# Kernel optimization log

Hardware: AMD Instinct MI355X
Metric: run time of the kernel (lower is better)

## Reference

```python
import jax, jax.numpy as jnp
import numpy as np

D_MODEL = 4096
RANK = 16
BATCH = 4
SEQ = 4096


def setup_inputs() -> dict:
    key = jax.random.key(0)
    k_x, k_w, k_b, k_a, k_bb = jax.random.split(key, 5)
    x = jax.random.normal(k_x, (BATCH, SEQ, D_MODEL), dtype=jnp.float32)
    W = jax.random.normal(k_w, (D_MODEL, D_MODEL), dtype=jnp.float32) * 0.02
    bias = jax.random.normal(k_b, (D_MODEL,), dtype=jnp.float32) * 0.02
    A = jax.random.normal(k_a, (D_MODEL, RANK), dtype=jnp.float32) * 0.01
    B = jax.random.normal(k_bb, (RANK, D_MODEL), dtype=jnp.float32) * 0.01
    return {"x": x, "W": W, "bias": bias, "A": A, "B": B}


def reference(x, W, bias, A, B):
    # Faithful to the torch module: delta_W = A @ B; linear(x, W + delta_W, bias)
    # i.e. out = x @ (W + A @ B)^T + bias, with W: [d_out, d_in], x: [b, s, d_in].
    delta_W = A @ B                                   # [d_out, d_in]
    out = jnp.einsum("bsi,oi->bso", x, W + delta_W) + bias
    return out
```

## Files before the change

kernel.cpp:

```cpp
#include <hip/hip_runtime.h>
#include <stdint.h>


#define MDIM 16384
#define NDIM 4096
#define KDIM 4096
#define RANK 16
#define NT   (KDIM / 64)

typedef __bf16  bf16x8 __attribute__((ext_vector_type(8)));
typedef float   f32x4  __attribute__((ext_vector_type(4)));
typedef unsigned short u16x8 __attribute__((ext_vector_type(8)));

__device__ __forceinline__ unsigned short f2bf(float f) {
  union { float f; uint32_t u; } v; v.f = f;
  uint32_t r = v.u + 0x7FFFu + ((v.u >> 16) & 1u);
  return (unsigned short)(r >> 16);
}

__device__ __forceinline__ void gl16(const void* g, void* l) {
  __builtin_amdgcn_global_load_lds(
      (__attribute__((address_space(1))) void*)(g),
      (__attribute__((address_space(3))) void*)(l),
      16, 0, 0);
}

__global__ void prep_w(const float* __restrict__ W, const float* __restrict__ A,
                       const float* __restrict__ Bm, unsigned short* __restrict__ Wp) {
  const int i = blockIdx.x * 256 + threadIdx.x;
  const int o = blockIdx.y;
  float acc = W[(size_t)o * NDIM + i];
#pragma unroll
  for (int r = 0; r < RANK; ++r)
    acc += A[o * RANK + r] * Bm[(size_t)r * NDIM + i];
  Wp[(size_t)o * NDIM + i] = f2bf(acc);
}

__global__ void cast_x(const float* __restrict__ x, unsigned short* __restrict__ xb) {
  const size_t i = ((size_t)blockIdx.x * 256 + threadIdx.x) * 8;
  float4 a = *(const float4*)(x + i);
  float4 b = *(const float4*)(x + i + 4);
  u16x8 o;
  o[0] = f2bf(a.x); o[1] = f2bf(a.y); o[2] = f2bf(a.z); o[3] = f2bf(a.w);
  o[4] = f2bf(b.x); o[5] = f2bf(b.y); o[6] = f2bf(b.z); o[7] = f2bf(b.w);
  *(u16x8*)(xb + i) = o;
}

#define BARRIER  __builtin_amdgcn_s_barrier()
#define VMCNT8   asm volatile("s_waitcnt vmcnt(8)" ::: "memory")
#define VMCNT6   asm volatile("s_waitcnt vmcnt(6)" ::: "memory")
#define WAITVM0  asm volatile("s_waitcnt vmcnt(0)" ::: "memory")

#define STAGE_A(buf, h, kt) do {                                              \
    const int kc_ = ((kt) < NT ? (kt) : NT - 1);                              \
    const unsigned short* g_ = agb + (size_t)((h) * 64) * KDIM + kc_ * 64;    \
    unsigned short* d_ = &sA[(buf)][0] + (h) * 8192 + t * 8;                  \
    gl16(g_, d_);                                                             \
    gl16(g_ + (size_t)128 * KDIM, d_ + 4096);                                 \
  } while (0)

#define STAGE_B(buf, h, kt) do {                                              \
    const int kc_ = ((kt) < NT ? (kt) : NT - 1);                              \
    const unsigned short* g_ = bgb + (size_t)((h) * 32) * KDIM + kc_ * 64;    \
    unsigned short* d_ = &sB[(buf)][0] + (h) * 8192 + t * 8;                  \
    gl16(g_, d_);                                                             \
    gl16(g_ + (size_t)128 * KDIM, d_ + 4096);                                 \
  } while (0)

#define LDA(buf, mh) do {                                                     \
    _Pragma("unroll") for (int mi = 0; mi < 4; ++mi)                          \
    _Pragma("unroll") for (int kk = 0; kk < 2; ++kk)                          \
      a[mi][kk] = *(const bf16x8*)(saw + (buf)*16384 + ((mh)*128 + mi*16)*64  \
                                   + ((kk*32 + koff) ^ xorE));                \
  } while (0)

#define LDB(buf, nh, bb) do {                                                 \
    _Pragma("unroll") for (int ni = 0; ni < 2; ++ni)                          \
    _Pragma("unroll") for (int kk = 0; kk < 2; ++kk)                          \
      bb[ni][kk] = *(const bf16x8*)(sbw + (buf)*16384 + ((nh)*128 + ni*16)*64 \
                                    + ((kk*32 + koff) ^ xorE));               \
  } while (0)

#define MM(mh, nh, bb) do {                                                   \
    __builtin_amdgcn_s_setprio(1);                                            \
    _Pragma("unroll") for (int mi = 0; mi < 4; ++mi)                          \
    _Pragma("unroll") for (int ni = 0; ni < 2; ++ni)                          \
    _Pragma("unroll") for (int kk = 0; kk < 2; ++kk)                          \
      acc[(mh)*4+mi][(nh)*2+ni] = __builtin_amdgcn_mfma_f32_16x16x32_bf16(    \
          a[mi][kk], bb[ni][kk], acc[(mh)*4+mi][(nh)*2+ni], 0, 0, 0);         \
    __builtin_amdgcn_s_setprio(0);                                            \
  } while (0)

__global__ __launch_bounds__(512, 2) void gemm256(
    const unsigned short* __restrict__ Xb,
    const unsigned short* __restrict__ Wp,
    const float* __restrict__ bias,
    float* __restrict__ out) {
  __shared__ __align__(16) unsigned short sA[2][256 * 64];
  __shared__ __align__(16) unsigned short sB[2][256 * 64];

  const int t  = threadIdx.x;
  const int l  = t & 63;
  const int w  = t >> 6;
  const int wm = w >> 2;
  const int wn = w & 3;

  const int bid = blockIdx.x;
  const int swz = (bid & 7) * (1024 / 8) + (bid >> 3);
  const int bm  = (swz >> 4) * 256;
  const int bn  = (swz & 15) * 256;

  const int sr  = t >> 3;
  const int ske = (((t & 7) * 16) ^ ((sr & 7) << 4)) >> 1;
  const unsigned short* agb = Xb + (size_t)(bm + sr) * KDIM + ske;
  const unsigned short* bgb = Wp + (size_t)(bn + (sr >> 5) * 64 + (sr & 31)) * KDIM + ske;

  const int lr   = l & 15;
  const int koff = (l >> 4) * 8;
  const int xorE = (lr & 7) << 3;
  const unsigned short* saw = &sA[0][0] + (wm * 64 + lr) * 64;
  const unsigned short* sbw = &sB[0][0] + (wn * 32 + lr) * 64;

  bf16x8 a[4][2], b0[2][2], b1[2][2];
  f32x4 acc[8][4];
#pragma unroll
  for (int i = 0; i < 8; ++i)
#pragma unroll
    for (int j = 0; j < 4; ++j)
      acc[i][j] = f32x4{0.f, 0.f, 0.f, 0.f};

  STAGE_A(0, 0, 0); STAGE_B(0, 0, 0); STAGE_A(0, 1, 0); STAGE_B(0, 1, 0);
  STAGE_A(1, 0, 1); STAGE_B(1, 0, 1); STAGE_B(1, 1, 1);
  VMCNT6;
  BARRIER;

  for (int it = 0; it < NT / 2; ++it) {
    const int E = it * 2;
    LDA(0, 0); LDB(0, 0, b0);
    STAGE_A(1, 1, E + 1);
    BARRIER;
    MM(0, 0, b0);
    BARRIER;
    LDB(0, 1, b1);
    STAGE_A(0, 0, E + 2);
    BARRIER;
    MM(0, 1, b1);
    VMCNT8;
    BARRIER;
    LDA(0, 1);
    STAGE_B(0, 0, E + 2);
    BARRIER;
    MM(1, 1, b1);
    BARRIER;
    STAGE_B(0, 1, E + 2);
    BARRIER;
    MM(1, 0, b0);
    VMCNT8;
    BARRIER;
    LDA(1, 0); LDB(1, 0, b0);
    STAGE_A(0, 1, E + 2);
    BARRIER;
    MM(0, 0, b0);
    BARRIER;
    LDB(1, 1, b1);
    STAGE_A(1, 0, E + 3);
    BARRIER;
    MM(0, 1, b1);
    VMCNT8;
    BARRIER;
    LDA(1, 1);
    STAGE_B(1, 0, E + 3);
    BARRIER;
    MM(1, 1, b1);
    BARRIER;
    STAGE_B(1, 1, E + 3);
    BARRIER;
    MM(1, 0, b0);
    VMCNT8;
    BARRIER;
  }

  WAITVM0;

#pragma unroll
  for (int mf = 0; mf < 8; ++mf) {
#pragma unroll
    for (int nf = 0; nf < 4; ++nf) {
      const int row = bm + wm * 128 + mf * 16 + (l >> 4) * 4;
      const int col = bn + wn * 64 + nf * 16 + lr;
      const float bv = bias[col];
#pragma unroll
      for (int r = 0; r < 4; ++r)
        out[(size_t)(row + r) * NDIM + col] = acc[mf][nf][r] + bv;
    }
  }
}

extern "C" void kernel_launch(void* const* d_in, const int* in_sizes, int n_in,
                              void* d_out, int out_size, void* d_ws, size_t ws_size,
                              hipStream_t stream) {
  const float* x    = (const float*)d_in[0];
  const float* W    = (const float*)d_in[1];
  const float* bias = (const float*)d_in[2];
  const float* A    = (const float*)d_in[3];
  const float* B    = (const float*)d_in[4];
  float* out        = (float*)d_out;

  unsigned short* Wp = (unsigned short*)d_ws;
  unsigned short* Xb = (unsigned short*)d_ws + (size_t)NDIM * KDIM;

  prep_w<<<dim3(NDIM / 256, NDIM), 256, 0, stream>>>(W, A, B, Wp);
  cast_x<<<dim3((size_t)MDIM * KDIM / (256 * 8)), 256, 0, stream>>>(x, Xb);
  gemm256<<<dim3((MDIM / 256) * (NDIM / 256)), 512, 0, stream>>>(Xb, Wp, bias, out);
}
```

Before: 634.1 us.

## Software-pipeline LDS fragment loads one quadrant ahead of MFMA with register double-buffering

Restructures the GEMM main loop so each shared-memory fragment load for the next quadrant is issued before the MFMA block that consumes the previous fragments. It uses extra register buffers (aA/aB, bX/bY/bZ) and sched_barriers, and re-times the global-to-LDS staging with uniform vmcnt(6) waits. The aim is to hide LDS read latency behind matrix math and remove the separate barrier-only phases. The cost is higher VGPR pressure, which may hurt occupancy under launch_bounds(512,2), plus some risk in the buffer-reuse ordering.

```diff
diff --git a/kernel.cpp b/kernel.cpp
--- a/kernel.cpp
+++ b/kernel.cpp
@@ -47,9 +47,10 @@
 }
 
 #define BARRIER  __builtin_amdgcn_s_barrier()
-#define VMCNT8   asm volatile("s_waitcnt vmcnt(8)" ::: "memory")
 #define VMCNT6   asm volatile("s_waitcnt vmcnt(6)" ::: "memory")
+#define VMCNT4   asm volatile("s_waitcnt vmcnt(4)" ::: "memory")
 #define WAITVM0  asm volatile("s_waitcnt vmcnt(0)" ::: "memory")
+#define SCHEDB   __builtin_amdgcn_sched_barrier(0)
 
 #define STAGE_A(buf, h, kt) do {                                              \
     const int kc_ = ((kt) < NT ? (kt) : NT - 1);                              \
@@ -67,27 +68,27 @@
     gl16(g_ + (size_t)128 * KDIM, d_ + 4096);                                 \
   } while (0)
 
-#define LDA(buf, mh) do {                                                     \
+#define LDA_TO(dst, buf, mh) do {                                             \
     _Pragma("unroll") for (int mi = 0; mi < 4; ++mi)                          \
     _Pragma("unroll") for (int kk = 0; kk < 2; ++kk)                          \
-      a[mi][kk] = *(const bf16x8*)(saw + (buf)*16384 + ((mh)*128 + mi*16)*64  \
-                                   + ((kk*32 + koff) ^ xorE));                \
-  } while (0)
-
-#define LDB(buf, nh, bb) do {                                                 \
+      dst[mi][kk] = *(const bf16x8*)(saw + (buf)*16384 + ((mh)*128 + mi*16)*64\
+                                     + ((kk*32 + koff) ^ xorE));              \
+  } while (0)
+
+#define LDB_TO(dst, buf, nh) do {                                             \
     _Pragma("unroll") for (int ni = 0; ni < 2; ++ni)                          \
     _Pragma("unroll") for (int kk = 0; kk < 2; ++kk)                          \
-      bb[ni][kk] = *(const bf16x8*)(sbw + (buf)*16384 + ((nh)*128 + ni*16)*64 \
-                                    + ((kk*32 + koff) ^ xorE));               \
-  } while (0)
-
-#define MM(mh, nh, bb) do {                                                   \
+      dst[ni][kk] = *(const bf16x8*)(sbw + (buf)*16384 + ((nh)*128 + ni*16)*64\
+                                     + ((kk*32 + koff) ^ xorE));              \
+  } while (0)
+
+#define MMQ(mh, nh, aS, bS) do {                                              \
     __builtin_amdgcn_s_setprio(1);                                            \
     _Pragma("unroll") for (int mi = 0; mi < 4; ++mi)                          \
     _Pragma("unroll") for (int ni = 0; ni < 2; ++ni)                          \
     _Pragma("unroll") for (int kk = 0; kk < 2; ++kk)                          \
       acc[(mh)*4+mi][(nh)*2+ni] = __builtin_amdgcn_mfma_f32_16x16x32_bf16(    \
-          a[mi][kk], bb[ni][kk], acc[(mh)*4+mi][(nh)*2+ni], 0, 0, 0);         \
+          aS[mi][kk], bS[ni][kk], acc[(mh)*4+mi][(nh)*2+ni], 0, 0, 0);        \
     __builtin_amdgcn_s_setprio(0);                                            \
   } while (0)
 
@@ -121,7 +122,7 @@
   const unsigned short* saw = &sA[0][0] + (wm * 64 + lr) * 64;
   const unsigned short* sbw = &sB[0][0] + (wn * 32 + lr) * 64;
 
-  bf16x8 a[4][2], b0[2][2], b1[2][2];
+  bf16x8 aA[4][2], aB[4][2], bX[2][2], bY[2][2], bZ[2][2];
   f32x4 acc[8][4];
 #pragma unroll
   for (int i = 0; i < 8; ++i)
@@ -129,55 +130,55 @@
     for (int j = 0; j < 4; ++j)
       acc[i][j] = f32x4{0.f, 0.f, 0.f, 0.f};
 
-  STAGE_A(0, 0, 0); STAGE_B(0, 0, 0); STAGE_A(0, 1, 0); STAGE_B(0, 1, 0);
-  STAGE_A(1, 0, 1); STAGE_B(1, 0, 1); STAGE_B(1, 1, 1);
-  VMCNT6;
+  STAGE_B(0, 0, 0); STAGE_A(0, 0, 0); STAGE_B(0, 1, 0); STAGE_A(0, 1, 0);
+  STAGE_B(1, 0, 1); STAGE_A(1, 0, 1);
+  VMCNT4;
   BARRIER;
+  LDB_TO(bX, 0, 0);
+  LDA_TO(aA, 0, 0);
 
   for (int it = 0; it < NT / 2; ++it) {
     const int E = it * 2;
-    LDA(0, 0); LDB(0, 0, b0);
+    LDB_TO(bY, 0, 1);
+    STAGE_B(1, 1, E + 1);
+    SCHEDB; BARRIER;
+    MMQ(0, 0, aA, bX);
+    VMCNT6; BARRIER;
+    LDA_TO(aB, 0, 1);
     STAGE_A(1, 1, E + 1);
-    BARRIER;
-    MM(0, 0, b0);
-    BARRIER;
-    LDB(0, 1, b1);
+    SCHEDB; BARRIER;
+    MMQ(0, 1, aA, bY);
+    VMCNT6; BARRIER;
+    LDB_TO(bZ, 1, 0);
+    STAGE_B(0, 0, E + 2);
+    SCHEDB; BARRIER;
+    MMQ(1, 1, aB, bY);
+    VMCNT6; BARRIER;
+    LDA_TO(aA, 1, 0);
     STAGE_A(0, 0, E + 2);
-    BARRIER;
-    MM(0, 1, b1);
-    VMCNT8;
-    BARRIER;
-    LDA(0, 1);
-    STAGE_B(0, 0, E + 2);
-    BARRIER;
-    MM(1, 1, b1);
-    BARRIER;
+    SCHEDB; BARRIER;
+    MMQ(1, 0, aB, bX);
+    VMCNT6; BARRIER;
+    LDB_TO(bY, 1, 1);
     STAGE_B(0, 1, E + 2);
-    BARRIER;
-    MM(1, 0, b0);
-    VMCNT8;
-    BARRIER;
-    LDA(1, 0); LDB(1, 0, b0);
+    SCHEDB; BARRIER;
+    MMQ(0, 0, aA, bZ);
+    VMCNT6; BARRIER;
+    LDA_TO(aB, 1, 1);
     STAGE_A(0, 1, E + 2);
-    BARRIER;
-    MM(0, 0, b0);
-    BARRIER;
-    LDB(1, 1, b1);
+    SCHEDB; BARRIER;
+    MMQ(0, 1, aA, bY);
+    VMCNT6; BARRIER;
+    LDB_TO(bX, 0, 0);
+    STAGE_B(1, 0, E + 3);
+    SCHEDB; BARRIER;
+    MMQ(1, 1, aB, bY);
+    VMCNT6; BARRIER;
+    LDA_TO(aA, 0, 0);
     STAGE_A(1, 0, E + 3);
-    BARRIER;
-    MM(0, 1, b1);
-    VMCNT8;
-    BARRIER;
-    LDA(1, 1);
-    STAGE_B(1, 0, E + 3);
-    BARRIER;
-    MM(1, 1, b1);
-    BARRIER;
-    STAGE_B(1, 1, E + 3);
-    BARRIER;
-    MM(1, 0, b0);
-    VMCNT8;
-    BARRIER;
+    SCHEDB; BARRIER;
+    MMQ(1, 0, aB, bZ);
+    VMCNT6; BARRIER;
   }
 
   WAITVM0;
```

Result: slower. 971.9 us (+53.3%).

## Switch GEMM to 32x32x16 MFMA and fuse weight prep with x cast

Applied to the files above, without the earlier changes.

Replaces the 16x16x32 bf16 MFMA tiles with 32x32x16 tiles, which changes the LDS fragment loads, the accumulator layout (f32x16) and the epilogue store mapping. The goal is fewer LDS reads per FLOP and fewer MFMA issues. It also merges the prep_w and cast_x kernels into one launch and vectorizes the weight-update path to 8 elements per thread. The risks are a different LDS bank-conflict pattern from the new XOR addressing and less coalesced epilogue stores.

```diff
diff --git a/kernel.cpp b/kernel.cpp
--- a/kernel.cpp
+++ b/kernel.cpp
@@ -9,7 +9,7 @@
 #define NT   (KDIM / 64)
 
 typedef __bf16  bf16x8 __attribute__((ext_vector_type(8)));
-typedef float   f32x4  __attribute__((ext_vector_type(4)));
+typedef float   f32x16 __attribute__((ext_vector_type(16)));
 typedef unsigned short u16x8 __attribute__((ext_vector_type(8)));
 
 __device__ __forceinline__ unsigned short f2bf(float f) {
@@ -25,25 +25,48 @@
       16, 0, 0);
 }
 
-__global__ void prep_w(const float* __restrict__ W, const float* __restrict__ A,
-                       const float* __restrict__ Bm, unsigned short* __restrict__ Wp) {
-  const int i = blockIdx.x * 256 + threadIdx.x;
-  const int o = blockIdx.y;
-  float acc = W[(size_t)o * NDIM + i];
-#pragma unroll
-  for (int r = 0; r < RANK; ++r)
-    acc += A[o * RANK + r] * Bm[(size_t)r * NDIM + i];
-  Wp[(size_t)o * NDIM + i] = f2bf(acc);
-}
-
-__global__ void cast_x(const float* __restrict__ x, unsigned short* __restrict__ xb) {
-  const size_t i = ((size_t)blockIdx.x * 256 + threadIdx.x) * 8;
-  float4 a = *(const float4*)(x + i);
-  float4 b = *(const float4*)(x + i + 4);
-  u16x8 o;
-  o[0] = f2bf(a.x); o[1] = f2bf(a.y); o[2] = f2bf(a.z); o[3] = f2bf(a.w);
-  o[4] = f2bf(b.x); o[5] = f2bf(b.y); o[6] = f2bf(b.z); o[7] = f2bf(b.w);
-  *(u16x8*)(xb + i) = o;
+#define CAST_BLOCKS 32768
+__global__ void prep_fused(const float* __restrict__ x,
+                           const float* __restrict__ W,
+                           const float* __restrict__ A,
+                           const float* __restrict__ Bm,
+                           unsigned short* __restrict__ xb,
+                           unsigned short* __restrict__ Wp) {
+  const int b = blockIdx.x;
+  if (b < CAST_BLOCKS) {
+    const size_t i = ((size_t)b * 256 + threadIdx.x) * 8;
+    float4 a0 = *(const float4*)(x + i);
+    float4 a1 = *(const float4*)(x + i + 4);
+    u16x8 o;
+    o[0] = f2bf(a0.x); o[1] = f2bf(a0.y); o[2] = f2bf(a0.z); o[3] = f2bf(a0.w);
+    o[4] = f2bf(a1.x); o[5] = f2bf(a1.y); o[6] = f2bf(a1.z); o[7] = f2bf(a1.w);
+    *(u16x8*)(xb + i) = o;
+  } else {
+    const size_t idx = ((size_t)(b - CAST_BLOCKS) * 256 + threadIdx.x) * 8;
+    const int o  = (int)(idx >> 12);
+    const int i0 = (int)(idx & 4095);
+    float accv[8];
+    {
+      float4 w0 = *(const float4*)(W + (size_t)o * NDIM + i0);
+      float4 w1 = *(const float4*)(W + (size_t)o * NDIM + i0 + 4);
+      accv[0] = w0.x; accv[1] = w0.y; accv[2] = w0.z; accv[3] = w0.w;
+      accv[4] = w1.x; accv[5] = w1.y; accv[6] = w1.z; accv[7] = w1.w;
+    }
+#pragma unroll
+    for (int r = 0; r < RANK; ++r) {
+      const float ar = A[o * RANK + r];
+      float4 b0 = *(const float4*)(Bm + (size_t)r * NDIM + i0);
+      float4 b1 = *(const float4*)(Bm + (size_t)r * NDIM + i0 + 4);
+      accv[0] += ar * b0.x; accv[1] += ar * b0.y;
+      accv[2] += ar * b0.z; accv[3] += ar * b0.w;
+      accv[4] += ar * b1.x; accv[5] += ar * b1.y;
+      accv[6] += ar * b1.z; accv[7] += ar * b1.w;
+    }
+    u16x8 ov;
+#pragma unroll
+    for (int j = 0; j < 8; ++j) ov[j] = f2bf(accv[j]);
+    *(u16x8*)(Wp + idx) = ov;
+  }
 }
 
 #define BARRIER  __builtin_amdgcn_s_barrier()
@@ -67,27 +90,36 @@
     gl16(g_ + (size_t)128 * KDIM, d_ + 4096);                                 \
   } while (0)
 
-#define LDA(buf, mh) do {                                                     \
-    _Pragma("unroll") for (int mi = 0; mi < 4; ++mi)                          \
-    _Pragma("unroll") for (int kk = 0; kk < 2; ++kk)                          \
-      a[mi][kk] = *(const bf16x8*)(saw + (buf)*16384 + ((mh)*128 + mi*16)*64  \
-                                   + ((kk*32 + koff) ^ xorE));                \
-  } while (0)
-
-#define LDB(buf, nh, bb) do {                                                 \
-    _Pragma("unroll") for (int ni = 0; ni < 2; ++ni)                          \
-    _Pragma("unroll") for (int kk = 0; kk < 2; ++kk)                          \
-      bb[ni][kk] = *(const bf16x8*)(sbw + (buf)*16384 + ((nh)*128 + ni*16)*64 \
-                                    + ((kk*32 + koff) ^ xorE));               \
-  } while (0)
-
-#define MM(mh, nh, bb) do {                                                   \
+#define LDA32(buf, mh) do {                                                   \
+    _Pragma("unroll") for (int mi = 0; mi < 2; ++mi)                          \
+    _Pragma("unroll") for (int ks = 0; ks < 4; ++ks)                          \
+      a[mi][ks] = *(const bf16x8*)(saw + (buf)*16384 + ((mh)*128 + mi*32)*64  \
+                                   + ((ks*16 + koff) ^ xorE));                \
+  } while (0)
+
+#define LDB32(dst, buf, nh) do {                                              \
+    _Pragma("unroll") for (int ks = 0; ks < 4; ++ks)                          \
+      dst[ks] = *(const bf16x8*)(sbw + (buf)*16384 + ((nh)*128)*64            \
+                                 + ((ks*16 + koff) ^ xorE));                  \
+  } while (0)
+
+#define LDAB32(buf, mh, nh, dst) do {                                         \
+    _Pragma("unroll") for (int ks = 0; ks < 4; ++ks) {                        \
+      dst[ks] = *(const bf16x8*)(sbw + (buf)*16384 + ((nh)*128)*64            \
+                                 + ((ks*16 + koff) ^ xorE));                  \
+      a[0][ks] = *(const bf16x8*)(saw + (buf)*16384 + ((mh)*128)*64           \
+                                  + ((ks*16 + koff) ^ xorE));                 \
+      a[1][ks] = *(const bf16x8*)(saw + (buf)*16384 + ((mh)*128 + 32)*64      \
+                                  + ((ks*16 + koff) ^ xorE));                 \
+    }                                                                         \
+  } while (0)
+
+#define MM32(mh, nh, bset) do {                                               \
     __builtin_amdgcn_s_setprio(1);                                            \
-    _Pragma("unroll") for (int mi = 0; mi < 4; ++mi)                          \
-    _Pragma("unroll") for (int ni = 0; ni < 2; ++ni)                          \
-    _Pragma("unroll") for (int kk = 0; kk < 2; ++kk)                          \
-      acc[(mh)*4+mi][(nh)*2+ni] = __builtin_amdgcn_mfma_f32_16x16x32_bf16(    \
-          a[mi][kk], bb[ni][kk], acc[(mh)*4+mi][(nh)*2+ni], 0, 0, 0);         \
+    _Pragma("unroll") for (int ks = 0; ks < 4; ++ks)                          \
+    _Pragma("unroll") for (int mi = 0; mi < 2; ++mi)                          \
+      acc[(mh)*2+mi][nh] = __builtin_amdgcn_mfma_f32_32x32x16_bf16(           \
+          a[mi][ks], bset[ks], acc[(mh)*2+mi][nh], 0, 0, 0);                  \
     __builtin_amdgcn_s_setprio(0);                                            \
   } while (0)
 
@@ -115,19 +147,21 @@
   const unsigned short* agb = Xb + (size_t)(bm + sr) * KDIM + ske;
   const unsigned short* bgb = Wp + (size_t)(bn + (sr >> 5) * 64 + (sr & 31)) * KDIM + ske;
 
-  const int lr   = l & 15;
-  const int koff = (l >> 4) * 8;
-  const int xorE = (lr & 7) << 3;
-  const unsigned short* saw = &sA[0][0] + (wm * 64 + lr) * 64;
-  const unsigned short* sbw = &sB[0][0] + (wn * 32 + lr) * 64;
-
-  bf16x8 a[4][2], b0[2][2], b1[2][2];
-  f32x4 acc[8][4];
-#pragma unroll
-  for (int i = 0; i < 8; ++i)
-#pragma unroll
-    for (int j = 0; j < 4; ++j)
-      acc[i][j] = f32x4{0.f, 0.f, 0.f, 0.f};
+  const int lc   = l & 31;
+  const int koff = (l >> 5) * 8;
+  const int xorE = (l & 7) << 3;
+  const unsigned short* saw = &sA[0][0] + (wm * 64 + lc) * 64;
+  const unsigned short* sbw = &sB[0][0] + (wn * 32 + lc) * 64;
+
+  bf16x8 a[2][4], b0[4], b1[4];
+  f32x16 acc[4][2];
+#pragma unroll
+  for (int i = 0; i < 4; ++i)
+#pragma unroll
+    for (int j = 0; j < 2; ++j)
+#pragma unroll
+      for (int r = 0; r < 16; ++r)
+        acc[i][j][r] = 0.f;
 
   STAGE_A(0, 0, 0); STAGE_B(0, 0, 0); STAGE_A(0, 1, 0); STAGE_B(0, 1, 0);
   STAGE_A(1, 0, 1); STAGE_B(1, 0, 1); STAGE_B(1, 1, 1);
@@ -136,62 +170,64 @@
 
   for (int it = 0; it < NT / 2; ++it) {
     const int E = it * 2;
-    LDA(0, 0); LDB(0, 0, b0);
+    LDAB32(0, 0, 0, b0);
     STAGE_A(1, 1, E + 1);
     BARRIER;
-    MM(0, 0, b0);
-    BARRIER;
-    LDB(0, 1, b1);
+    MM32(0, 0, b0);
+    BARRIER;
+    LDB32(b1, 0, 1);
     STAGE_A(0, 0, E + 2);
     BARRIER;
-    MM(0, 1, b1);
-    VMCNT8;
-    BARRIER;
-    LDA(0, 1);
+    MM32(0, 1, b1);
+    VMCNT8;
+    BARRIER;
+    LDA32(0, 1);
     STAGE_B(0, 0, E + 2);
     BARRIER;
-    MM(1, 1, b1);
+    MM32(1, 1, b1);
     BARRIER;
     STAGE_B(0, 1, E + 2);
     BARRIER;
-    MM(1, 0, b0);
-    VMCNT8;
-    BARRIER;
-    LDA(1, 0); LDB(1, 0, b0);
+    MM32(1, 0, b0);
+    VMCNT8;
+    BARRIER;
+    LDAB32(1, 0, 0, b0);
     STAGE_A(0, 1, E + 2);
     BARRIER;
-    MM(0, 0, b0);
-    BARRIER;
-    LDB(1, 1, b1);
+    MM32(0, 0, b0);
+    BARRIER;
+    LDB32(b1, 1, 1);
     STAGE_A(1, 0, E + 3);
     BARRIER;
-    MM(0, 1, b1);
-    VMCNT8;
-    BARRIER;
-    LDA(1, 1);
+    MM32(0, 1, b1);
+    VMCNT8;
+    BARRIER;
+    LDA32(1, 1);
     STAGE_B(1, 0, E + 3);
     BARRIER;
-    MM(1, 1, b1);
+    MM32(1, 1, b1);
     BARRIER;
     STAGE_B(1, 1, E + 3);
     BARRIER;
-    MM(1, 0, b0);
+    MM32(1, 0, b0);
     VMCNT8;
     BARRIER;
   }
 
   WAITVM0;
 
-#pragma unroll
-  for (int mf = 0; mf < 8; ++mf) {
-#pragma unroll
-    for (int nf = 0; nf < 4; ++nf) {
-      const int row = bm + wm * 128 + mf * 16 + (l >> 4) * 4;
-      const int col = bn + wn * 64 + nf * 16 + lr;
-      const float bv = bias[col];
-#pragma unroll
-      for (int r = 0; r < 4; ++r)
-        out[(size_t)(row + r) * NDIM + col] = acc[mf][nf][r] + bv;
+  const int rbase = bm + wm * 128 + 4 * (l >> 5);
+#pragma unroll
+  for (int nf = 0; nf < 2; ++nf) {
+    const int col = bn + wn * 64 + nf * 32 + lc;
+    const float bv = bias[col];
+#pragma unroll
+    for (int mf = 0; mf < 4; ++mf) {
+#pragma unroll
+      for (int reg = 0; reg < 16; ++reg) {
+        const int row = rbase + mf * 32 + (reg & 3) + 8 * (reg >> 2);
+        out[(size_t)row * NDIM + col] = acc[mf][nf][reg] + bv;
+      }
     }
   }
 }
@@ -209,7 +245,6 @@
   unsigned short* Wp = (unsigned short*)d_ws;
   unsigned short* Xb = (unsigned short*)d_ws + (size_t)NDIM * KDIM;
 
-  prep_w<<<dim3(NDIM / 256, NDIM), 256, 0, stream>>>(W, A, B, Wp);
-  cast_x<<<dim3((size_t)MDIM * KDIM / (256 * 8)), 256, 0, stream>>>(x, Xb);
+  prep_fused<<<dim3(CAST_BLOCKS + 8192), 256, 0, stream>>>(x, W, A, B, Xb, Wp);
   gemm256<<<dim3((MDIM / 256) * (NDIM / 256)), 512, 0, stream>>>(Xb, Wp, bias, out);
 }
```

Result: slower. 708.0 us (+11.6%).

## Fuse weight prep and x cast into one launch; use inline-asm LDS reads

Applied to the files above, without the earlier changes.

Merges the W+A@B bf16 prep kernel and the x-to-bf16 cast into a single launch, with the weight part vectorised to eight elements per thread. This removes one kernel launch and gap and cuts scalar loads in the weight prep. In the GEMM, LDS fragment loads become inline-asm ds_read_b128 with precomputed base addresses and immediate offsets, followed by an explicit lgkmcnt(0) wait and a scheduling barrier before each MFMA block. That cuts address arithmetic, but the forced waits and pinned schedule may reduce overlap between LDS reads and MFMA work.

```diff
diff --git a/kernel.cpp b/kernel.cpp
--- a/kernel.cpp
+++ b/kernel.cpp
@@ -25,31 +25,60 @@
       16, 0, 0);
 }
 
-__global__ void prep_w(const float* __restrict__ W, const float* __restrict__ A,
-                       const float* __restrict__ Bm, unsigned short* __restrict__ Wp) {
-  const int i = blockIdx.x * 256 + threadIdx.x;
-  const int o = blockIdx.y;
-  float acc = W[(size_t)o * NDIM + i];
-#pragma unroll
-  for (int r = 0; r < RANK; ++r)
-    acc += A[o * RANK + r] * Bm[(size_t)r * NDIM + i];
-  Wp[(size_t)o * NDIM + i] = f2bf(acc);
-}
-
-__global__ void cast_x(const float* __restrict__ x, unsigned short* __restrict__ xb) {
-  const size_t i = ((size_t)blockIdx.x * 256 + threadIdx.x) * 8;
-  float4 a = *(const float4*)(x + i);
-  float4 b = *(const float4*)(x + i + 4);
-  u16x8 o;
-  o[0] = f2bf(a.x); o[1] = f2bf(a.y); o[2] = f2bf(a.z); o[3] = f2bf(a.w);
-  o[4] = f2bf(b.x); o[5] = f2bf(b.y); o[6] = f2bf(b.z); o[7] = f2bf(b.w);
-  *(u16x8*)(xb + i) = o;
+#define CAST_BLOCKS 32768
+__global__ void prep_fused(const float* __restrict__ x,
+                           const float* __restrict__ W,
+                           const float* __restrict__ A,
+                           const float* __restrict__ Bm,
+                           unsigned short* __restrict__ xb,
+                           unsigned short* __restrict__ Wp) {
+  const int b = blockIdx.x;
+  if (b < CAST_BLOCKS) {
+    const size_t i = ((size_t)b * 256 + threadIdx.x) * 8;
+    float4 a0 = *(const float4*)(x + i);
+    float4 a1 = *(const float4*)(x + i + 4);
+    u16x8 o;
+    o[0] = f2bf(a0.x); o[1] = f2bf(a0.y); o[2] = f2bf(a0.z); o[3] = f2bf(a0.w);
+    o[4] = f2bf(a1.x); o[5] = f2bf(a1.y); o[6] = f2bf(a1.z); o[7] = f2bf(a1.w);
+    *(u16x8*)(xb + i) = o;
+  } else {
+    const size_t idx = ((size_t)(b - CAST_BLOCKS) * 256 + threadIdx.x) * 8;
+    const int o  = (int)(idx >> 12);
+    const int i0 = (int)(idx & 4095);
+    float accv[8];
+    {
+      float4 w0 = *(const float4*)(W + (size_t)o * NDIM + i0);
+      float4 w1 = *(const float4*)(W + (size_t)o * NDIM + i0 + 4);
+      accv[0] = w0.x; accv[1] = w0.y; accv[2] = w0.z; accv[3] = w0.w;
+      accv[4] = w1.x; accv[5] = w1.y; accv[6] = w1.z; accv[7] = w1.w;
+    }
+#pragma unroll
+    for (int r = 0; r < RANK; ++r) {
+      const float ar = A[o * RANK + r];
+      float4 b0 = *(const float4*)(Bm + (size_t)r * NDIM + i0);
+      float4 b1 = *(const float4*)(Bm + (size_t)r * NDIM + i0 + 4);
+      accv[0] += ar * b0.x; accv[1] += ar * b0.y;
+      accv[2] += ar * b0.z; accv[3] += ar * b0.w;
+      accv[4] += ar * b1.x; accv[5] += ar * b1.y;
+      accv[6] += ar * b1.z; accv[7] += ar * b1.w;
+    }
+    u16x8 ov;
+#pragma unroll
+    for (int j = 0; j < 8; ++j) ov[j] = f2bf(accv[j]);
+    *(u16x8*)(Wp + idx) = ov;
+  }
 }
 
 #define BARRIER  __builtin_amdgcn_s_barrier()
 #define VMCNT8   asm volatile("s_waitcnt vmcnt(8)" ::: "memory")
 #define VMCNT6   asm volatile("s_waitcnt vmcnt(6)" ::: "memory")
 #define WAITVM0  asm volatile("s_waitcnt vmcnt(0)" ::: "memory")
+#define LGKM0    asm volatile("s_waitcnt lgkmcnt(0)" ::: "memory")
+#define SCHEDB   __builtin_amdgcn_sched_barrier(0)
+
+#define DSR(dst, addr, imm)                                                   \
+  asm volatile("ds_read_b128 %0, %1 offset:%c2"                               \
+               : "=v"(dst) : "v"(addr), "n"(imm) : "memory")
 
 #define STAGE_A(buf, h, kt) do {                                              \
     const int kc_ = ((kt) < NT ? (kt) : NT - 1);                              \
@@ -68,17 +97,21 @@
   } while (0)
 
 #define LDA(buf, mh) do {                                                     \
-    _Pragma("unroll") for (int mi = 0; mi < 4; ++mi)                          \
-    _Pragma("unroll") for (int kk = 0; kk < 2; ++kk)                          \
-      a[mi][kk] = *(const bf16x8*)(saw + (buf)*16384 + ((mh)*128 + mi*16)*64  \
-                                   + ((kk*32 + koff) ^ xorE));                \
-  } while (0)
-
-#define LDB(buf, nh, bb) do {                                                 \
-    _Pragma("unroll") for (int ni = 0; ni < 2; ++ni)                          \
-    _Pragma("unroll") for (int kk = 0; kk < 2; ++kk)                          \
-      bb[ni][kk] = *(const bf16x8*)(sbw + (buf)*16384 + ((nh)*128 + ni*16)*64 \
-                                    + ((kk*32 + koff) ^ xorE));               \
+    DSR(a[0][0], aAddr0, (buf)*32768 + (mh)*16384 + 0);                       \
+    DSR(a[0][1], aAddr1, (buf)*32768 + (mh)*16384 + 0);                       \
+    DSR(a[1][0], aAddr0, (buf)*32768 + (mh)*16384 + 2048);                    \
+    DSR(a[1][1], aAddr1, (buf)*32768 + (mh)*16384 + 2048);                    \
+    DSR(a[2][0], aAddr0, (buf)*32768 + (mh)*16384 + 4096);                    \
+    DSR(a[2][1], aAddr1, (buf)*32768 + (mh)*16384 + 4096);                    \
+    DSR(a[3][0], aAddr0, (buf)*32768 + (mh)*16384 + 6144);                    \
+    DSR(a[3][1], aAddr1, (buf)*32768 + (mh)*16384 + 6144);                    \
+  } while (0)
+
+#define LDB(bb, buf, nh) do {                                                 \
+    DSR(bb[0][0], bAddr0, (buf)*32768 + (nh)*16384 + 0);                      \
+    DSR(bb[0][1], bAddr1, (buf)*32768 + (nh)*16384 + 0);                      \
+    DSR(bb[1][0], bAddr0, (buf)*32768 + (nh)*16384 + 2048);                   \
+    DSR(bb[1][1], bAddr1, (buf)*32768 + (nh)*16384 + 2048);                   \
   } while (0)
 
 #define MM(mh, nh, bb) do {                                                   \
@@ -118,8 +151,12 @@
   const int lr   = l & 15;
   const int koff = (l >> 4) * 8;
   const int xorE = (lr & 7) << 3;
-  const unsigned short* saw = &sA[0][0] + (wm * 64 + lr) * 64;
-  const unsigned short* sbw = &sB[0][0] + (wn * 32 + lr) * 64;
+  const unsigned ldsA = (unsigned)(uintptr_t)&sA[0][0];
+  const unsigned ldsB = (unsigned)(uintptr_t)&sB[0][0];
+  const unsigned aAddr0 = ldsA + (unsigned)((wm * 64 + lr) * 128 + ((koff ^ xorE) * 2));
+  const unsigned aAddr1 = ldsA + (unsigned)((wm * 64 + lr) * 128 + (((32 + koff) ^ xorE) * 2));
+  const unsigned bAddr0 = ldsB + (unsigned)((wn * 32 + lr) * 128 + ((koff ^ xorE) * 2));
+  const unsigned bAddr1 = ldsB + (unsigned)((wn * 32 + lr) * 128 + (((32 + koff) ^ xorE) * 2));
 
   bf16x8 a[4][2], b0[2][2], b1[2][2];
   f32x4 acc[8][4];
@@ -136,20 +173,20 @@
 
   for (int it = 0; it < NT / 2; ++it) {
     const int E = it * 2;
-    LDA(0, 0); LDB(0, 0, b0);
+    LDA(0, 0); LDB(b0, 0, 0);
     STAGE_A(1, 1, E + 1);
-    BARRIER;
+    BARRIER; LGKM0; SCHEDB;
     MM(0, 0, b0);
     BARRIER;
-    LDB(0, 1, b1);
+    LDB(b1, 0, 1);
     STAGE_A(0, 0, E + 2);
-    BARRIER;
+    BARRIER; LGKM0; SCHEDB;
     MM(0, 1, b1);
     VMCNT8;
     BARRIER;
     LDA(0, 1);
     STAGE_B(0, 0, E + 2);
-    BARRIER;
+    BARRIER; LGKM0; SCHEDB;
     MM(1, 1, b1);
     BARRIER;
     STAGE_B(0, 1, E + 2);
@@ -157,20 +194,20 @@
     MM(1, 0, b0);
     VMCNT8;
     BARRIER;
-    LDA(1, 0); LDB(1, 0, b0);
+    LDA(1, 0); LDB(b0, 1, 0);
     STAGE_A(0, 1, E + 2);
-    BARRIER;
+    BARRIER; LGKM0; SCHEDB;
     MM(0, 0, b0);
     BARRIER;
-    LDB(1, 1, b1);
+    LDB(b1, 1, 1);
     STAGE_A(1, 0, E + 3);
-    BARRIER;
+    BARRIER; LGKM0; SCHEDB;
     MM(0, 1, b1);
     VMCNT8;
     BARRIER;
     LDA(1, 1);
     STAGE_B(1, 0, E + 3);
-    BARRIER;
+    BARRIER; LGKM0; SCHEDB;
     MM(1, 1, b1);
     BARRIER;
     STAGE_B(1, 1, E + 3);
@@ -209,7 +246,6 @@
   unsigned short* Wp = (unsigned short*)d_ws;
   unsigned short* Xb = (unsigned short*)d_ws + (size_t)NDIM * KDIM;
 
-  prep_w<<<dim3(NDIM / 256, NDIM), 256, 0, stream>>>(W, A, B, Wp);
-  cast_x<<<dim3((size_t)MDIM * KDIM / (256 * 8)), 256, 0, stream>>>(x, Xb);
+  prep_fused<<<dim3(CAST_BLOCKS + 8192), 256, 0, stream>>>(x, W, A, B, Xb, Wp);
   gemm256<<<dim3((MDIM / 256) * (NDIM / 256)), 512, 0, stream>>>(Xb, Wp, bias, out);
 }
```

After: 596.2 us. -6.0%, faster.
